# Performance work log

Hardware: AMD Instinct MI355X
Metric: run time of the kernel (lower is better)

## Reference

```python
import jax, jax.numpy as jnp
import numpy as np

B, T, D = 2, 2048, 4096
H, HKV, HD = 32, 8, 128
N_REP = H // HKV
THETA = 500000.0


def _rope(x, cos, sin):
    # x: [B, T, h, HD]; cos/sin: [T, HD//2]
    xr = x.reshape(*x.shape[:-1], HD // 2, 2)
    x0, x1 = xr[..., 0], xr[..., 1]
    c = cos[None, :, None, :]
    s = sin[None, :, None, :]
    o0 = x0 * c - x1 * s
    o1 = x0 * s + x1 * c
    return jnp.stack([o0, o1], axis=-1).reshape(x.shape)


def setup_inputs() -> dict:
    key = jax.random.key(0)
    ks = jax.random.split(key, 8)
    x = jax.random.normal(ks[0], (B, T, D), dtype=jnp.float32)
    # true Llama RoPE angles
    inv_freq = 1.0 / (THETA ** (np.arange(0, HD, 2, dtype=np.float32) / HD))
    ang = np.outer(np.arange(T, dtype=np.float32), inv_freq)  # [T, HD//2]
    freqs_cos = jnp.asarray(np.cos(ang), dtype=jnp.float32)
    freqs_sin = jnp.asarray(np.sin(ang), dtype=jnp.float32)
    mask = jnp.zeros((T, T), dtype=jnp.float32)  # accepted but unused (as in source)
    cache_k = jnp.zeros((B, T, HKV, HD), dtype=jnp.float32)
    cache_v = jnp.zeros((B, T, HKV, HD), dtype=jnp.float32)
    sc = 0.02
    wq = jax.random.normal(ks[1], (D, H * HD), dtype=jnp.float32) * sc
    wk = jax.random.normal(ks[2], (D, HKV * HD), dtype=jnp.float32) * sc
    wv = jax.random.normal(ks[3], (D, HKV * HD), dtype=jnp.float32) * sc
    wo = jax.random.normal(ks[4], (H * HD, D), dtype=jnp.float32) * sc
    return {"x": x, "freqs_cos": freqs_cos, "freqs_sin": freqs_sin, "mask": mask,
            "cache_k": cache_k, "cache_v": cache_v,
            "wq": wq, "wk": wk, "wv": wv, "wo": wo, "start_pos": 0}


def reference(x, freqs_cos, freqs_sin, mask, cache_k, cache_v, wq, wk, wv, wo, start_pos):
    b, t, _ = x.shape
    q = (x @ wq).reshape(b, t, H, HD)
    k = (x @ wk).reshape(b, t, HKV, HD)
    v = (x @ wv).reshape(b, t, HKV, HD)
    q = _rope(q, freqs_cos, freqs_sin)
    k = _rope(k, freqs_cos, freqs_sin)
    # KV-cache write
    cache_k = jax.lax.dynamic_update_slice(cache_k, k, (0, start_pos, 0, 0))
    cache_v = jax.lax.dynamic_update_slice(cache_v, v, (0, start_pos, 0, 0))
    s_len = start_pos + t
    keys = jnp.repeat(cache_k[:, :s_len], N_REP, axis=2)    # [B, S, H, HD]
    values = jnp.repeat(cache_v[:, :s_len], N_REP, axis=2)  # [B, S, H, HD]
    # per-head scaled dot-product attention (vectorized over heads)
    scores = jnp.einsum('bthd,bshd->bhts', q, keys) / jnp.sqrt(jnp.float32(HD))
    probs = jax.nn.softmax(scores, axis=-1)  # mask is NOT applied in the source forward
    out = jnp.einsum('bhts,bshd->bthd', probs, values).reshape(b, t, H * HD)
    return out @ wo
```

## Files before the change

### kernel.cpp

```cpp
#include <hip/hip_runtime.h>

typedef unsigned short u16;
typedef unsigned int   u32;
typedef __attribute__((ext_vector_type(2))) unsigned int u32x2;
typedef __attribute__((ext_vector_type(4))) float f32x4;
typedef __attribute__((ext_vector_type(8))) short s16x8;
typedef __attribute__((ext_vector_type(4))) _Float16 f16x4;
typedef __attribute__((ext_vector_type(8))) _Float16 f16x8;

#define B_   2
#define T_   2048
#define D_   4096
#define H_   32
#define HKV_ 8
#define HD_  128
#define NQKV 6144
#define M_   (B_*T_)

__device__ __forceinline__ u16 f2bf(float f){
  u32 u = __float_as_uint(f);
  u += 0x7fffu + ((u >> 16) & 1u);
  return (u16)(u >> 16);
}
__device__ __forceinline__ float bf2f(u16 h){
  return __uint_as_float(((u32)h) << 16);
}
__device__ __forceinline__ void gload16(const void* g, void* l){
  __builtin_amdgcn_global_load_lds(
      (const __attribute__((address_space(1))) u32*)g,
      (__attribute__((address_space(3))) u32*)l, 16, 0, 0);
}

__global__ void k_convert_x(const float* __restrict__ in, u16* __restrict__ out){
  int i = blockIdx.x * 256 + threadIdx.x;
  float4 v = reinterpret_cast<const float4*>(in)[i];
  u32 lo = (u32)f2bf(v.x) | ((u32)f2bf(v.y) << 16);
  u32 hi = (u32)f2bf(v.z) | ((u32)f2bf(v.w) << 16);
  u32x2 p; p.x = lo; p.y = hi;
  reinterpret_cast<u32x2*>(out)[i] = p;
}

__global__ void k_transpose_w(const float* __restrict__ in, u16* __restrict__ out,
                              int K, int N){
  __shared__ float tile[64][65];
  int n0 = blockIdx.x * 64, k0 = blockIdx.y * 64;
  int tid = threadIdx.x;
  int tx = tid & 15, ty = tid >> 4;
  #pragma unroll
  for (int rr = 0; rr < 4; rr++) {
    int r = ty + 16 * rr;
    float4 v = *reinterpret_cast<const float4*>(in + (size_t)(k0 + r) * N + n0 + 4 * tx);
    tile[r][4 * tx + 0] = v.x; tile[r][4 * tx + 1] = v.y;
    tile[r][4 * tx + 2] = v.z; tile[r][4 * tx + 3] = v.w;
  }
  __syncthreads();
  #pragma unroll
  for (int ni = 0; ni < 4; ni++) {
    int nn = ty + 16 * ni;
    ushort4 o;
    o.x = f2bf(tile[4 * tx + 0][nn]);
    o.y = f2bf(tile[4 * tx + 1][nn]);
    o.z = f2bf(tile[4 * tx + 2][nn]);
    o.w = f2bf(tile[4 * tx + 3][nn]);
    *reinterpret_cast<ushort4*>(out + (size_t)(n0 + nn) * K + k0 + 4 * tx) = o;
  }
}

template<int OUT_F32>
__global__ __launch_bounds__(256, 2) void k_gemm(
    const u16* __restrict__ A, const u16* __restrict__ Bt,
    void* __restrict__ Cv, int M, int N, int K)
{
  __shared__ __attribute__((aligned(16))) unsigned char smem[32768];
  unsigned char* As = smem;
  unsigned char* Bs = smem + 16384;
  const int tid = threadIdx.x;
  const int w = tid >> 6, l = tid & 63;
  const int m0 = blockIdx.y * 128, n0 = blockIdx.x * 128;
  const int wm = (w >> 1) * 64, wn = (w & 1) * 64;
  f32x4 acc[4][4];
  #pragma unroll
  for (int i = 0; i < 4; i++)
    #pragma unroll
    for (int j = 0; j < 4; j++)
      acc[i][j] = f32x4{0.f, 0.f, 0.f, 0.f};

  const int srcoff = 8 * ((l & 7) ^ ((l >> 3) & 7));
  const int subrow = l >> 3;

  for (int k0 = 0; k0 < K; k0 += 64) {
    if (k0) __syncthreads();
    #pragma unroll
    for (int i = 0; i < 4; i++) {
      int chunk = 4 * w + i;
      int row = chunk * 8 + subrow;
      gload16(A  + (size_t)(m0 + row) * K + k0 + srcoff, As + chunk * 1024);
      gload16(Bt + (size_t)(n0 + row) * K + k0 + srcoff, Bs + chunk * 1024);
    }
    asm volatile("s_waitcnt vmcnt(0)" ::: "memory");
    __syncthreads();
    #pragma unroll
    for (int kk = 0; kk < 2; kk++) {
      s16x8 a[4], b[4];
      const int co = kk * 64 + 16 * (l >> 4);
      #pragma unroll
      for (int mi = 0; mi < 4; mi++) {
        int r = wm + 16 * mi + (l & 15);
        a[mi] = *reinterpret_cast<const s16x8*>(As + r * 128 + (co ^ ((r & 7) << 4)));
      }
      #pragma unroll
      for (int ni = 0; ni < 4; ni++) {
        int r = wn + 16 * ni + (l & 15);
        b[ni] = *reinterpret_cast<const s16x8*>(Bs + r * 128 + (co ^ ((r & 7) << 4)));
      }
      #pragma unroll
      for (int mi = 0; mi < 4; mi++)
        #pragma unroll
        for (int ni = 0; ni < 4; ni++)
          acc[mi][ni] = __builtin_amdgcn_mfma_f32_16x16x32_bf16(a[mi], b[ni], acc[mi][ni], 0, 0, 0);
    }
  }
  const int g = l >> 4, c = l & 15;
  #pragma unroll
  for (int mi = 0; mi < 4; mi++)
    #pragma unroll
    for (int ni = 0; ni < 4; ni++)
      #pragma unroll
      for (int r = 0; r < 4; r++) {
        int m = m0 + wm + 16 * mi + 4 * g + r;
        int n = n0 + wn + 16 * ni + c;
        float v = acc[mi][ni][r];
        if (OUT_F32) reinterpret_cast<float*>(Cv)[(size_t)m * N + n] = v;
        else         reinterpret_cast<u16*>(Cv)[(size_t)m * N + n] = f2bf(v);
      }
}

__global__ void k_rope_q(u16* C1, const float* __restrict__ fc, const float* __restrict__ fs){
  int idx = blockIdx.x * 256 + threadIdx.x;
  int m = idx >> 11, p = idx & 2047;
  int h = p >> 6, i = p & 63;
  int t = m & (T_ - 1);
  u32* ptr = reinterpret_cast<u32*>(C1 + (size_t)m * NQKV + h * HD_ + 2 * i);
  u32 u = *ptr;
  float x0 = __uint_as_float(u << 16);
  float x1 = __uint_as_float(u & 0xffff0000u);
  float cc = fc[t * 64 + i], ss = fs[t * 64 + i];
  float o0 = x0 * cc - x1 * ss;
  float o1 = x0 * ss + x1 * cc;
  *ptr = (u32)f2bf(o0) | ((u32)f2bf(o1) << 16);
}

__global__ void k_rope_k(const u16* __restrict__ C1, const float* __restrict__ fc,
                         const float* __restrict__ fs, unsigned char* __restrict__ Kg){
  int idx = blockIdx.x * 256 + threadIdx.x;
  int m = idx >> 9, p = idx & 511;
  int kh = p >> 6, i = p & 63;
  int b = m >> 11, t = m & (T_ - 1);
  u32 u = *reinterpret_cast<const u32*>(C1 + (size_t)m * NQKV + D_ + kh * HD_ + 2 * i);
  float x0 = __uint_as_float(u << 16);
  float x1 = __uint_as_float(u & 0xffff0000u);
  float cc = fc[t * 64 + i], ss = fs[t * 64 + i];
  float o0 = x0 * cc - x1 * ss;
  float o1 = x0 * ss + x1 * cc;
  u32 packed = (u32)f2bf(o0) | ((u32)f2bf(o1) << 16);
  unsigned char* Kbb = Kg + (size_t)(b * HKV_ + kh) * 524288;
  int swb = (((i >> 2) ^ (t & 7)) << 4) | (4 * (i & 3));
  *reinterpret_cast<u32*>(Kbb + (size_t)t * 256 + swb) = packed;
}

__global__ void k_v_trans(const u16* __restrict__ C1, unsigned char* __restrict__ Vg){
  __shared__ float tile[32][33];
  int bz = blockIdx.z;
  int t0 = blockIdx.x * 32, d0 = blockIdx.y * 32;
  int tx = threadIdx.x, ty = threadIdx.y;
  int b = bz >> 3, kh = bz & 7;
  const u16* src = C1 + (size_t)(b * T_) * NQKV + D_ + HKV_ * HD_ + kh * HD_;
  #pragma unroll
  for (int i = ty; i < 32; i += 8)
    tile[i][tx] = bf2f(src[(size_t)(t0 + i) * NQKV + d0 + tx]);
  __syncthreads();
  unsigned char* Vbb = Vg + (size_t)bz * 524288;
  #pragma unroll
  for (int i = ty; i < 32; i += 8) {
    int d = d0 + i;
    int k = t0 + tx;
    int tt = k >> 6, kv = k & 63;
    int pp = (kv & 0x23) | ((kv & 0x10) >> 2) | ((kv & 0x0C) << 1);
    int swb = (((pp >> 3) ^ (d & 7)) << 4) | (2 * (pp & 7));
    *reinterpret_cast<_Float16*>(Vbb + (size_t)tt * 16384 + d * 128 + swb) =
        (_Float16)tile[tx][i];
  }
}

__global__ __launch_bounds__(256, 2) void k_attn(
    const u16* __restrict__ Q,
    const unsigned char* __restrict__ Kg,
    const unsigned char* __restrict__ Vg,
    u16* __restrict__ Ob)
{
  __shared__ __attribute__((aligned(16))) unsigned char smem[65536];
  const int tid = threadIdx.x;
  const int w = tid >> 6, l = tid & 63;
  const int c = l & 15, g = l >> 4;
  const int q0 = blockIdx.x * 128 + w * 32;
  const int h = blockIdx.y, b = blockIdx.z;
  const int kh = h >> 2;
  const unsigned char* Kb_ = Kg + (size_t)(b * HKV_ + kh) * 524288;
  const unsigned char* Vb_ = Vg + (size_t)(b * HKV_ + kh) * 524288;

  const float SCL2 = 0.08838834764831845f * 1.4426950408889634f;
  const float OFF2 = 14.4269504f;

  s16x8 qf[2][4];
  #pragma unroll
  for (int qt = 0; qt < 2; qt++)
    #pragma unroll
    for (int ci = 0; ci < 4; ci++)
      qf[qt][ci] = *reinterpret_cast<const s16x8*>(
          Q + (size_t)(b * T_ + q0 + 16 * qt + c) * NQKV + h * HD_ + 32 * ci + 8 * g);

  f32x4 o[2][8];
  #pragma unroll
  for (int qt = 0; qt < 2; qt++)
    #pragma unroll
    for (int i = 0; i < 8; i++) o[qt][i] = f32x4{0.f, 0.f, 0.f, 0.f};
  float lsum[2] = {0.f, 0.f};

  auto stage = [&](int bi, int tt) {
    const unsigned char* Ks = Kb_ + (size_t)tt * 16384;
    const unsigned char* Vs = Vb_ + (size_t)tt * 16384;
    unsigned char* Kl = smem + bi * 32768;
    unsigned char* Vl = Kl + 16384;
    #pragma unroll
    for (int i = 0; i < 4; i++) {
      int ch = i * 4 + w;
      gload16(Ks + ch * 1024 + l * 16, Kl + ch * 1024);
      gload16(Vs + ch * 1024 + l * 16, Vl + ch * 1024);
    }
  };

  stage(0, 0);
  asm volatile("s_waitcnt vmcnt(0)" ::: "memory");
  __syncthreads();

  for (int tt = 0; tt < T_ / 64; ++tt) {
    int cur = tt & 1;
    if (tt < T_ / 64 - 1) stage(cur ^ 1, tt + 1);
    const unsigned char* Kl = smem + cur * 32768;
    const unsigned char* Vl = Kl + 16384;

    f32x4 s[4][2];
    #pragma unroll
    for (int mi = 0; mi < 4; mi++)
      #pragma unroll
      for (int qt = 0; qt < 2; qt++) s[mi][qt] = f32x4{0.f, 0.f, 0.f, 0.f};

    #pragma unroll
    for (int mi = 0; mi < 4; mi++) {
      const int row = 16 * mi + c;
      const int sw = (row & 7) << 4;
      s16x8 kf[4];
      #pragma unroll
      for (int ci = 0; ci < 4; ci++)
        kf[ci] = *reinterpret_cast<const s16x8*>(Kl + row * 256 + ((64 * ci + 16 * g) ^ sw));
      #pragma unroll
      for (int qt = 0; qt < 2; qt++)
        #pragma unroll
        for (int ci = 0; ci < 4; ci++)
          s[mi][qt] = __builtin_amdgcn_mfma_f32_16x16x32_bf16(kf[ci], qf[qt][ci], s[mi][qt], 0, 0, 0);
    }

    f16x4 pa[2][4];
    #pragma unroll
    for (int qt = 0; qt < 2; qt++)
      #pragma unroll
      for (int mi = 0; mi < 4; mi++)
        #pragma unroll
        for (int r = 0; r < 4; r++) {
          float p = exp2f(s[mi][qt][r] * SCL2 - OFF2);
          lsum[qt] += p;
          pa[qt][mi][r] = (_Float16)p;
        }

    #pragma unroll
    for (int cp = 0; cp < 2; cp++)
      #pragma unroll
      for (int dc = 0; dc < 8; dc++) {
        const int d = 16 * dc + c;
        f16x8 v8 = *reinterpret_cast<const f16x8*>(
            Vl + d * 128 + ((64 * cp + 16 * g) ^ ((d & 7) << 4)));
        f16x4 lo = {v8[0], v8[1], v8[2], v8[3]};
        f16x4 hi = {v8[4], v8[5], v8[6], v8[7]};
        #pragma unroll
        for (int qt = 0; qt < 2; qt++) {
          o[qt][dc] = __builtin_amdgcn_mfma_f32_16x16x16f16(pa[qt][2 * cp], lo, o[qt][dc], 0, 0, 0);
          o[qt][dc] = __builtin_amdgcn_mfma_f32_16x16x16f16(pa[qt][2 * cp + 1], hi, o[qt][dc], 0, 0, 0);
        }
      }

    asm volatile("s_waitcnt vmcnt(0)" ::: "memory");
    __syncthreads();
  }

  #pragma unroll
  for (int qt = 0; qt < 2; qt++) {
    lsum[qt] += __shfl_xor(lsum[qt], 16);
    lsum[qt] += __shfl_xor(lsum[qt], 32);
  }
  float inv[2][4];
  #pragma unroll
  for (int qt = 0; qt < 2; qt++)
    #pragma unroll
    for (int r = 0; r < 4; r++)
      inv[qt][r] = 1.0f / __shfl(lsum[qt], 4 * g + r, 64);

  #pragma unroll
  for (int qt = 0; qt < 2; qt++) {
    u16* Orow = Ob + (size_t)(b * T_ + q0 + 16 * qt) * D_ + h * HD_;
    #pragma unroll
    for (int dc = 0; dc < 8; dc++)
      #pragma unroll
      for (int r = 0; r < 4; r++)
        Orow[(size_t)(4 * g + r) * D_ + 16 * dc + c] = f2bf(o[qt][dc][r] * inv[qt][r]);
  }
}

extern "C" void kernel_launch(void* const* d_in, const int* in_sizes, int n_in,
                              void* d_out, int out_size, void* d_ws, size_t ws_size,
                              hipStream_t stream)
{
  const float* x  = (const float*)d_in[0];
  const float* fc = (const float*)d_in[1];
  const float* fs = (const float*)d_in[2];
  const float* wq = (const float*)d_in[6];
  const float* wk = (const float*)d_in[7];
  const float* wv = (const float*)d_in[8];
  const float* wo = (const float*)d_in[9];

  unsigned char* w = (unsigned char*)d_ws;
  u16* Xb   = (u16*)(w);
  u16* Wt   = (u16*)(w + 33554432ull);
  u16* Wot  = (u16*)(w + 83886080ull);
  u16* C1   = (u16*)(w + 117440512ull);
  unsigned char* Kg = w + 167772160ull;
  unsigned char* Vg = w + 176160768ull;
  u16* Ob   = (u16*)(w + 184549376ull);

  k_convert_x<<<16384, 256, 0, stream>>>(x, Xb);
  k_transpose_w<<<dim3(64, 64), 256, 0, stream>>>(wq, Wt, D_, D_);
  k_transpose_w<<<dim3(16, 64), 256, 0, stream>>>(wk, Wt + (size_t)D_ * D_, D_, 1024);
  k_transpose_w<<<dim3(16, 64), 256, 0, stream>>>(wv, Wt + (size_t)5120 * D_, D_, 1024);
  k_transpose_w<<<dim3(64, 64), 256, 0, stream>>>(wo, Wot, D_, D_);

  k_gemm<0><<<dim3(NQKV / 128, M_ / 128), 256, 0, stream>>>(Xb, Wt, C1, M_, NQKV, D_);

  k_rope_q<<<32768, 256, 0, stream>>>(C1, fc, fs);
  k_rope_k<<<8192, 256, 0, stream>>>(C1, fc, fs, Kg);
  k_v_trans<<<dim3(64, 4, 16), dim3(32, 8), 0, stream>>>(C1, Vg);

  k_attn<<<dim3(T_ / 128, H_, B_), 256, 0, stream>>>(C1, Kg, Vg, Ob);

  k_gemm<1><<<dim3(D_ / 128, M_ / 128), 256, 0, stream>>>(Ob, Wot, d_out, M_, D_, D_);
}
```

Baseline: 602.2 us.

## Replace GEMM with 256x256-tile, 8-wave, double-buffered pipelined kernel

Replaces the 128x128 single-buffered bf16 MFMA GEMM with a 256x256 tile kernel using 8 waves and 128KB of LDS split into two buffers. Global-to-LDS loads for the next K-tile are interleaved with MFMA phases, with partial vmcnt waits, explicit barriers and s_setprio. Workgroup IDs are remapped across blocks to improve L2 locality. The goal is to hide memory latency and raise data reuse per block. The cost is one block per CU, high register pressure from 32 accumulators, and tighter tile divisibility assumptions.

```diff
diff --git a/kernel.cpp b/kernel.cpp
--- a/kernel.cpp
+++ b/kernel.cpp
@@ -66,69 +66,115 @@
   }
 }
 
+#define AS_(b) (smem + (b) * 65536)
+#define BS_(b) (smem + (b) * 65536 + 32768)
+#define BARX  asm volatile("s_barrier" ::: "memory")
+#define PRIO1 __builtin_amdgcn_s_setprio(1)
+#define PRIO0 __builtin_amdgcn_s_setprio(0)
+#define VM4   asm volatile("s_waitcnt vmcnt(4)" ::: "memory")
+#define VM0   asm volatile("s_waitcnt vmcnt(0)" ::: "memory")
+#define LGKM0 do { asm volatile("s_waitcnt lgkmcnt(0)" ::: "memory"); \
+                   __builtin_amdgcn_sched_barrier(0); } while (0)
+
+#define STAGE_HA(buf, half, kt) { \
+  _Pragma("unroll") for (int r2 = 0; r2 < 2; r2++) { \
+    int rw = (half) * 128 + r2 * 64 + w * 8; \
+    gload16(A + (size_t)(m0 + rw + subrow) * K + (kt) * 64 + srcoff, \
+            AS_(buf) + rw * 128); } }
+#define STAGE_HB(buf, half, kt) { \
+  _Pragma("unroll") for (int r2 = 0; r2 < 2; r2++) { \
+    int rw = (half) * 128 + r2 * 64 + w * 8; \
+    gload16(Bt + (size_t)(n0 + rw + subrow) * K + (kt) * 64 + srcoff, \
+            BS_(buf) + rw * 128); } }
+#define RD_A2(buf, p) { \
+  _Pragma("unroll") for (int rt = 0; rt < 2; rt++) { \
+    int row = wr * 128 + (p) * 32 + rt * 16 + c; \
+    const unsigned char* ptr = AS_(buf) + row * 128; \
+    int sw = (row & 7) << 4; \
+    af[rt][0] = *(const s16x8*)(ptr + ((16 * g) ^ sw)); \
+    af[rt][1] = *(const s16x8*)(ptr + ((64 + 16 * g) ^ sw)); } }
+#define RD_B8(buf) { \
+  _Pragma("unroll") for (int ni = 0; ni < 4; ni++) { \
+    int row = wc * 64 + ni * 16 + c; \
+    const unsigned char* ptr = BS_(buf) + row * 128; \
+    int sw = (row & 7) << 4; \
+    bfr[ni][0] = *(const s16x8*)(ptr + ((16 * g) ^ sw)); \
+    bfr[ni][1] = *(const s16x8*)(ptr + ((64 + 16 * g) ^ sw)); } }
+#define MFP(p) { \
+  _Pragma("unroll") for (int rt = 0; rt < 2; rt++) \
+  _Pragma("unroll") for (int ni = 0; ni < 4; ni++) \
+  _Pragma("unroll") for (int kk = 0; kk < 2; kk++) \
+    acc[(p) * 2 + rt][ni] = __builtin_amdgcn_mfma_f32_16x16x32_bf16( \
+        af[rt][kk], bfr[ni][kk], acc[(p) * 2 + rt][ni], 0, 0, 0); }
+
 template<int OUT_F32>
-__global__ __launch_bounds__(256, 2) void k_gemm(
+__global__ __launch_bounds__(512, 1) void k_gemm8(
     const u16* __restrict__ A, const u16* __restrict__ Bt,
     void* __restrict__ Cv, int M, int N, int K)
 {
-  __shared__ __attribute__((aligned(16))) unsigned char smem[32768];
-  unsigned char* As = smem;
-  unsigned char* Bs = smem + 16384;
+  __shared__ __attribute__((aligned(16))) unsigned char smem[131072];
   const int tid = threadIdx.x;
   const int w = tid >> 6, l = tid & 63;
-  const int m0 = blockIdx.y * 128, n0 = blockIdx.x * 128;
-  const int wm = (w >> 1) * 64, wn = (w & 1) * 64;
-  f32x4 acc[4][4];
-  #pragma unroll
-  for (int i = 0; i < 4; i++)
+  const int c = l & 15, g = l >> 4;
+  const int wr = w >> 2, wc = w & 3;
+
+  const int nbx = N >> 8;
+  const int nwg = nbx * (M >> 8);
+  const int orig = blockIdx.x;
+  const int id = (orig & 7) * (nwg >> 3) + (orig >> 3);
+  const int m0 = (id / nbx) << 8;
+  const int n0 = (id % nbx) << 8;
+
+  const int srcoff = 8 * ((l & 7) ^ ((l >> 3) & 7));
+  const int subrow = l >> 3;
+
+  f32x4 acc[8][4];
+  #pragma unroll
+  for (int i = 0; i < 8; i++)
     #pragma unroll
     for (int j = 0; j < 4; j++)
       acc[i][j] = f32x4{0.f, 0.f, 0.f, 0.f};
-
-  const int srcoff = 8 * ((l & 7) ^ ((l >> 3) & 7));
-  const int subrow = l >> 3;
-
-  for (int k0 = 0; k0 < K; k0 += 64) {
-    if (k0) __syncthreads();
-    #pragma unroll
-    for (int i = 0; i < 4; i++) {
-      int chunk = 4 * w + i;
-      int row = chunk * 8 + subrow;
-      gload16(A  + (size_t)(m0 + row) * K + k0 + srcoff, As + chunk * 1024);
-      gload16(Bt + (size_t)(n0 + row) * K + k0 + srcoff, Bs + chunk * 1024);
-    }
-    asm volatile("s_waitcnt vmcnt(0)" ::: "memory");
-    __syncthreads();
-    #pragma unroll
-    for (int kk = 0; kk < 2; kk++) {
-      s16x8 a[4], b[4];
-      const int co = kk * 64 + 16 * (l >> 4);
-      #pragma unroll
-      for (int mi = 0; mi < 4; mi++) {
-        int r = wm + 16 * mi + (l & 15);
-        a[mi] = *reinterpret_cast<const s16x8*>(As + r * 128 + (co ^ ((r & 7) << 4)));
-      }
-      #pragma unroll
-      for (int ni = 0; ni < 4; ni++) {
-        int r = wn + 16 * ni + (l & 15);
-        b[ni] = *reinterpret_cast<const s16x8*>(Bs + r * 128 + (co ^ ((r & 7) << 4)));
-      }
-      #pragma unroll
-      for (int mi = 0; mi < 4; mi++)
-        #pragma unroll
-        for (int ni = 0; ni < 4; ni++)
-          acc[mi][ni] = __builtin_amdgcn_mfma_f32_16x16x32_bf16(a[mi], b[ni], acc[mi][ni], 0, 0, 0);
-    }
-  }
-  const int g = l >> 4, c = l & 15;
-  #pragma unroll
-  for (int mi = 0; mi < 4; mi++)
+  s16x8 af[2][2], bfr[4][2];
+
+  STAGE_HB(0, 0, 0); STAGE_HB(0, 1, 0);
+  STAGE_HA(0, 0, 0); STAGE_HA(0, 1, 0);
+  STAGE_HB(1, 0, 1); STAGE_HB(1, 1, 1);
+  VM4; BARX;
+
+  const int NT2 = K >> 7;
+  for (int it = 0; it < NT2; ++it) {
+    const int tA = 2 * it, tB = 2 * it + 1;
+    const bool st = (it < NT2 - 1);
+    RD_A2(0, 0); RD_B8(0); STAGE_HA(1, 0, tB);
+    BARX; LGKM0; PRIO1; MFP(0); PRIO0; BARX;
+    RD_A2(0, 1); STAGE_HA(1, 1, tB);
+    BARX; LGKM0; PRIO1; MFP(1); PRIO0; BARX;
+    RD_A2(0, 2); if (st) STAGE_HB(0, 0, tA + 2);
+    BARX; LGKM0; PRIO1; MFP(2); PRIO0; BARX;
+    RD_A2(0, 3); if (st) STAGE_HB(0, 1, tA + 2);
+    BARX; LGKM0; PRIO1; MFP(3); PRIO0;
+    if (st) { VM4; } else { VM0; }
+    BARX;
+    RD_A2(1, 0); RD_B8(1); if (st) STAGE_HA(0, 0, tA + 2);
+    BARX; LGKM0; PRIO1; MFP(0); PRIO0; BARX;
+    RD_A2(1, 1); if (st) STAGE_HA(0, 1, tA + 2);
+    BARX; LGKM0; PRIO1; MFP(1); PRIO0; BARX;
+    RD_A2(1, 2); if (st) STAGE_HB(1, 0, tB + 2);
+    BARX; LGKM0; PRIO1; MFP(2); PRIO0; BARX;
+    RD_A2(1, 3); if (st) STAGE_HB(1, 1, tB + 2);
+    BARX; LGKM0; PRIO1; MFP(3); PRIO0;
+    if (st) { VM4; }
+    BARX;
+  }
+
+  #pragma unroll
+  for (int mi = 0; mi < 8; mi++)
     #pragma unroll
     for (int ni = 0; ni < 4; ni++)
       #pragma unroll
       for (int r = 0; r < 4; r++) {
-        int m = m0 + wm + 16 * mi + 4 * g + r;
-        int n = n0 + wn + 16 * ni + c;
+        int m = m0 + wr * 128 + 16 * mi + 4 * g + r;
+        int n = n0 + wc * 64 + 16 * ni + c;
         float v = acc[mi][ni][r];
         if (OUT_F32) reinterpret_cast<float*>(Cv)[(size_t)m * N + n] = v;
         else         reinterpret_cast<u16*>(Cv)[(size_t)m * N + n] = f2bf(v);
@@ -352,7 +398,7 @@
   k_transpose_w<<<dim3(16, 64), 256, 0, stream>>>(wv, Wt + (size_t)5120 * D_, D_, 1024);
   k_transpose_w<<<dim3(64, 64), 256, 0, stream>>>(wo, Wot, D_, D_);
 
-  k_gemm<0><<<dim3(NQKV / 128, M_ / 128), 256, 0, stream>>>(Xb, Wt, C1, M_, NQKV, D_);
+  k_gemm8<0><<<(NQKV / 256) * (M_ / 256), 512, 0, stream>>>(Xb, Wt, C1, M_, NQKV, D_);
 
   k_rope_q<<<32768, 256, 0, stream>>>(C1, fc, fs);
   k_rope_k<<<8192, 256, 0, stream>>>(C1, fc, fs, Kg);
@@ -360,5 +406,5 @@
 
   k_attn<<<dim3(T_ / 128, H_, B_), 256, 0, stream>>>(C1, Kg, Vg, Ob);
 
-  k_gemm<1><<<dim3(D_ / 128, M_ / 128), 256, 0, stream>>>(Ob, Wot, d_out, M_, D_, D_);
-}
+  k_gemm8<1><<<(D_ / 256) * (M_ / 256), 512, 0, stream>>>(Ob, Wot, d_out, M_, D_, D_);
+}
```

Measured after the change: 579.1 us. -3.8%, faster.
